# Kernel tuning notes

Hardware: AMD Instinct MI355X
Metric: run time of the kernel (lower is better)

Reference implementation:

```python
import jax, jax.numpy as jnp
import numpy as np

TAU = 2.0       # spikingjelly LIFNode default
V_TH = 1.0      # v_threshold default
ALPHA = 2.0     # surrogate.ATan default alpha

@jax.custom_vjp
def atan_spike(x):
    # Heaviside forward, ATan surrogate gradient backward
    return (x >= 0.0).astype(x.dtype)

def _atan_fwd(x):
    return atan_spike(x), x

def _atan_bwd(x, g):
    return (g * (ALPHA / 2.0) / (1.0 + (jnp.pi / 2.0 * ALPHA * x) ** 2),)

atan_spike.defvjp(_atan_fwd, _atan_bwd)

def lif_scan(cur):
    # cur: [T, ...]; LIF with decay_input=True, hard reset to v_reset=0
    def step(v, c):
        v = v + (c - v) / TAU          # charge with decayed input
        s = atan_spike(v - V_TH)       # fire
        v = (1.0 - s) * v              # hard reset (v_reset = 0)
        return v, s
    v0 = jnp.zeros(cur.shape[1:], cur.dtype)
    _, spikes = jax.lax.scan(step, v0, cur)
    return spikes

def setup_inputs() -> dict:
    key = jax.random.key(0)
    k1, k2 = jax.random.split(key, 2)
    T, B, D = 2048, 32, 512
    x = jax.random.normal(k1, (T, B, D), dtype=jnp.float32)
    W = jax.random.normal(k2, (D, D), dtype=jnp.float32) / np.sqrt(D).astype(np.float32)
    b = jnp.zeros((D,), dtype=jnp.float32)
    return {"x": x, "W": W, "b": b}

def reference(x, W, b):
    # x: [T, B, D]
    xs = jnp.stack([x, jnp.flip(x, axis=0)], axis=2)          # [T, B, 2, D]
    cur = jnp.einsum('tbkd,ed->tbke', xs, W) + b              # Linear (y = x W^T + b)
    s = lif_scan(cur)                                          # [T, B, 2, D] spikes
    return s[:, :, 0, :] + jnp.flip(s[:, :, 1, :], axis=0)    # [T, B, D]
```

## Files before the change

kernel.cpp:

```cpp
#include <hip/hip_runtime.h>
#include <cstddef>
#include <cstdint>

#define T_LEN 2048
#define B_SZ  32
#define D_SZ  512
#define BD    (B_SZ * D_SZ)

#define BM   128
#define BN   128

typedef const __attribute__((address_space(1))) uint32_t* gas1_t;
typedef __attribute__((address_space(3))) uint32_t* las3_t;

__global__ __launch_bounds__(256) void gemm8x8_kernel(
    const float* __restrict__ A,
    const float* __restrict__ W,
    const float* __restrict__ bias,
    float* __restrict__ Y)
{
#pragma clang fp contract(off)
  __shared__ float As[2][BM * 16];
  __shared__ float Bs[2][BN * 16];

  const int tid = threadIdx.x;
  const int tx  = tid & 15;
  const int ty  = tid >> 4;
  const int cA  = ty & 3;
  const int cB  = (tx >> 1) & 3;

  const int nwg  = (int)(gridDim.x * gridDim.y);
  const int orig = (int)(blockIdx.y * gridDim.x + blockIdx.x);
  const int q    = nwg >> 3, r = nwg & 7;
  const int xcd  = orig & 7, loc = orig >> 3;
  const int tix  = (xcd < r ? xcd * (q + 1) : r * (q + 1) + (xcd - r) * q) + loc;
  const int m0   = (tix >> 2) * BM;
  const int n0   = (tix & 3) * BN;

  const int lane  = tid & 63;
  const int wid   = tid >> 6;
  const int rloc  = lane >> 2;
  const int qA4   = (((lane & 3) ^ (rloc & 3)) << 2);
  const int qB4   = (((lane & 3) ^ ((rloc >> 1) & 3)) << 2);
  const int s0    = 2 * wid, s1 = 2 * wid + 1;
  const int oS0   = s0 * 256, oS1 = s1 * 256;
  const float* gA0 = A + (size_t)(m0 + s0 * 16 + rloc) * D_SZ + qA4;
  const float* gA1 = A + (size_t)(m0 + s1 * 16 + rloc) * D_SZ + qA4;
  const float* gB0 = W + (size_t)(n0 + s0 * 16 + rloc) * D_SZ + qB4;
  const float* gB1 = W + (size_t)(n0 + s1 * 16 + rloc) * D_SZ + qB4;

#define STAGE(BUF, KOFF)                                                      \
  do {                                                                        \
    __builtin_amdgcn_global_load_lds((gas1_t)(const void*)(gA0 + (KOFF)),     \
                                     (las3_t)(void*)(&As[BUF][oS0]), 16, 0, 0);\
    __builtin_amdgcn_global_load_lds((gas1_t)(const void*)(gA1 + (KOFF)),     \
                                     (las3_t)(void*)(&As[BUF][oS1]), 16, 0, 0);\
    __builtin_amdgcn_global_load_lds((gas1_t)(const void*)(gB0 + (KOFF)),     \
                                     (las3_t)(void*)(&Bs[BUF][oS0]), 16, 0, 0);\
    __builtin_amdgcn_global_load_lds((gas1_t)(const void*)(gB1 + (KOFF)),     \
                                     (las3_t)(void*)(&Bs[BUF][oS1]), 16, 0, 0);\
  } while (0)

  float acc[8][8];
#pragma unroll
  for (int i = 0; i < 8; ++i)
#pragma unroll
    for (int j = 0; j < 8; ++j) acc[i][j] = 0.0f;

  STAGE(0, 0);
  __syncthreads();

#pragma unroll 1
  for (int kc = 0; kc < 32; ++kc) {
    const int cur = kc & 1;
    if (kc + 1 < 32) STAGE(cur ^ 1, (kc + 1) * 16);

    const float* asb = &As[cur][0];
    const float* bsb = &Bs[cur][0];
#pragma unroll
    for (int kq = 0; kq < 4; ++kq) {
      const int bq = ((kq ^ cB) & 3) << 2;
      const int aq = ((kq ^ cA) & 3) << 2;
      float4 bfr[8];
#pragma unroll
      for (int j = 0; j < 8; ++j)
        bfr[j] = *(const float4*)&bsb[(tx + 16 * j) * 16 + bq];
#pragma unroll
      for (int i = 0; i < 8; ++i) {
        const float4 a = *(const float4*)&asb[(ty + 16 * i) * 16 + aq];
#pragma unroll
        for (int j = 0; j < 8; ++j) {
          acc[i][j] = fmaf(a.x, bfr[j].x, acc[i][j]);
          acc[i][j] = fmaf(a.y, bfr[j].y, acc[i][j]);
          acc[i][j] = fmaf(a.z, bfr[j].z, acc[i][j]);
          acc[i][j] = fmaf(a.w, bfr[j].w, acc[i][j]);
        }
      }
    }
    __syncthreads();
  }
#undef STAGE

#pragma unroll
  for (int i = 0; i < 8; ++i) {
    const int m = m0 + ty + 16 * i;
#pragma unroll
    for (int j = 0; j < 8; ++j) {
      const int n = n0 + tx + 16 * j;
      Y[(size_t)m * D_SZ + n] = acc[i][j] + bias[n];
    }
  }
}

#define CHK  16
#define CLEN 128

__global__ __launch_bounds__(64) void scan_chunk_kernel(
    const float* __restrict__ Y,
    float* __restrict__ out)
{
#pragma clang fp contract(off)
  const int idx = blockIdx.x * 64 + threadIdx.x;
  const int c   = blockIdx.y;
  const int t0  = c * CLEN;
  float ca[32], cb[32];
  uint32_t sf0, sf1, sf2, sf3, sb0, sb1, sb2, sb3;
  float v;

#define LD(R, TB)                                                             \
  _Pragma("unroll")                                                           \
  for (int j = 0; j < 32; ++j) R[j] = Y[(size_t)((TB) + j) * BD + idx];

#define FCH(R, W)                                                             \
  {                                                                           \
    uint32_t w_ = 0;                                                          \
    _Pragma("unroll")                                                         \
    for (int j = 0; j < 32; ++j) {                                            \
      v = v + (R[j] - v) * 0.5f;                                              \
      const bool s = (v - 1.0f) >= 0.0f;                                      \
      w_ |= (uint32_t)s << j;                                                 \
      v = s ? 0.0f : v;                                                       \
    }                                                                         \
    W = w_;                                                                   \
  }

#define BCH(R, W)                                                             \
  {                                                                           \
    uint32_t w_ = 0;                                                          \
    _Pragma("unroll")                                                         \
    for (int j = 31; j >= 0; --j) {                                           \
      v = v + (R[j] - v) * 0.5f;                                              \
      const bool s = (v - 1.0f) >= 0.0f;                                      \
      w_ |= (uint32_t)s << j;                                                 \
      v = s ? 0.0f : v;                                                       \
    }                                                                         \
    W = w_;                                                                   \
  }

  uint32_t wdump;

  v = 0.0f;
  if (c > 0) {
    LD(ca, t0 - 64)
    LD(cb, t0 - 32)
    FCH(ca, wdump)
    LD(ca, t0)
    FCH(cb, wdump)
  } else {
    LD(ca, t0)
  }
  LD(cb, t0 + 32)  FCH(ca, sf0)
  LD(ca, t0 + 64)  FCH(cb, sf1)
  LD(cb, t0 + 96)  FCH(ca, sf2)
                   FCH(cb, sf3)

  v = 0.0f;
  if (c < CHK - 1) {
    LD(ca, t0 + CLEN + 32)
    LD(cb, t0 + CLEN)
    BCH(ca, wdump)
    LD(ca, t0 + 96)
    BCH(cb, wdump)
  } else {
    LD(ca, t0 + 96)
  }
  LD(cb, t0 + 64)  BCH(ca, sb3)
  LD(ca, t0 + 32)  BCH(cb, sb2)
  LD(cb, t0)       BCH(ca, sb1)
                   BCH(cb, sb0)

#define WGRP(SF, SB, G)                                                       \
  _Pragma("unroll")                                                           \
  for (int j = 0; j < 32; ++j)                                                \
    out[(size_t)(t0 + (G) * 32 + j) * BD + idx] =                             \
        (float)(((SF >> j) & 1u) + ((SB >> j) & 1u));
  WGRP(sf0, sb0, 0) WGRP(sf1, sb1, 1) WGRP(sf2, sb2, 2) WGRP(sf3, sb3, 3)

#undef LD
#undef FCH
#undef BCH
#undef WGRP
}

__global__ __launch_bounds__(64) void lif_fwd_kernel(
    const float* __restrict__ Y, float* __restrict__ out,
    int tlen, float* __restrict__ vstate, int carry)
{
#pragma clang fp contract(off)
  const int idx = blockIdx.x * 64 + threadIdx.x;
  float v = carry ? vstate[idx] : 0.0f;
#pragma unroll 16
  for (int t = 0; t < tlen; ++t) {
    const float c = Y[(size_t)t * BD + idx];
    v = v + (c - v) * 0.5f;
    const bool s = (v - 1.0f) >= 0.0f;
    out[(size_t)t * BD + idx] = s ? 1.0f : 0.0f;
    v = s ? 0.0f : v;
  }
  vstate[idx] = v;
}

__global__ __launch_bounds__(64) void lif_bwd_kernel(
    const float* __restrict__ Y, float* __restrict__ out,
    int tlen, float* __restrict__ vstate, int carry)
{
#pragma clang fp contract(off)
  const int idx = blockIdx.x * 64 + threadIdx.x;
  float v = carry ? vstate[idx] : 0.0f;
#pragma unroll 16
  for (int tt = 0; tt < tlen; ++tt) {
    const size_t t = (size_t)(tlen - 1 - tt);
    const float c = Y[t * BD + idx];
    v = v + (c - v) * 0.5f;
    const bool s = (v - 1.0f) >= 0.0f;
    out[t * BD + idx] += s ? 1.0f : 0.0f;
    v = s ? 0.0f : v;
  }
  vstate[idx] = v;
}

extern "C" void kernel_launch(void* const* d_in, const int* in_sizes, int n_in,
                              void* d_out, int out_size, void* d_ws, size_t ws_size,
                              hipStream_t stream)
{
  const float* x = (const float*)d_in[0];
  const float* W = (const float*)d_in[1];
  const float* b = (const float*)d_in[2];
  float* out = (float*)d_out;

  const size_t full_bytes = (size_t)T_LEN * BD * sizeof(float);
  const size_t vbytes     = (size_t)BD * sizeof(float);

  if (ws_size >= full_bytes) {
    float* Y = (float*)d_ws;
    dim3 grid(T_LEN * B_SZ / BM, D_SZ / BN);
    gemm8x8_kernel<<<grid, 256, 0, stream>>>(x, W, b, Y);
    scan_chunk_kernel<<<dim3(BD / 64, CHK), 64, 0, stream>>>(Y, out);
  } else {
    const size_t avail = ws_size > vbytes ? ws_size - vbytes : 0;
    int Tc = T_LEN;
    while (Tc > 4 && (size_t)Tc * BD * sizeof(float) > avail) Tc >>= 1;
    float* Y      = (float*)d_ws;
    float* vstate = (float*)((char*)d_ws + (size_t)Tc * BD * sizeof(float));

    int first = 1;
    for (int t0 = 0; t0 < T_LEN; t0 += Tc) {
      dim3 grid(Tc * B_SZ / BM, D_SZ / BN);
      gemm8x8_kernel<<<grid, 256, 0, stream>>>(x + (size_t)t0 * BD, W, b, Y);
      lif_fwd_kernel<<<BD / 64, 64, 0, stream>>>(Y, out + (size_t)t0 * BD, Tc,
                                                 vstate, first ? 0 : 1);
      first = 0;
    }
    first = 1;
    for (int t0 = T_LEN - Tc; t0 >= 0; t0 -= Tc) {
      dim3 grid(Tc * B_SZ / BM, D_SZ / BN);
      gemm8x8_kernel<<<grid, 256, 0, stream>>>(x + (size_t)t0 * BD, W, b, Y);
      lif_bwd_kernel<<<BD / 64, 64, 0, stream>>>(Y, out + (size_t)t0 * BD, Tc,
                                                 vstate, first ? 0 : 1);
      first = 0;
    }
  }
}
```

Measured before the change: 650.2 us.

## Process two columns per thread with float2 loads and halve scan chunk length

The chunked LIF scan now has each thread handle two adjacent columns using float2 loads and stores, and the chunk length drops from 128 to 64 steps with twice as many chunks. The warm-up stays at 64 steps, so the redundant warm-up work grows relative to the useful work per chunk. The aim is wider memory transactions and two independent recurrences per thread for instruction-level parallelism. The cost is more redundant warm-up reads and higher register use.

```diff
diff --git a/kernel.cpp b/kernel.cpp
--- a/kernel.cpp
+++ b/kernel.cpp
@@ -112,94 +112,143 @@
   }
 }
 
-#define CHK  16
-#define CLEN 128
+#define CHK  32
+#define CLEN 64
 
 __global__ __launch_bounds__(64) void scan_chunk_kernel(
     const float* __restrict__ Y,
     float* __restrict__ out)
 {
 #pragma clang fp contract(off)
-  const int idx = blockIdx.x * 64 + threadIdx.x;
+  const int col = (blockIdx.x * 64 + threadIdx.x) * 2;
   const int c   = blockIdx.y;
   const int t0  = c * CLEN;
-  float ca[32], cb[32];
-  uint32_t sf0, sf1, sf2, sf3, sb0, sb1, sb2, sb3;
-  float v;
+  float2 ca[16], cb[16];
+  uint32_t sfx0, sfx1, sfy0, sfy1;
+  float vx, vy;
 
 #define LD(R, TB)                                                             \
   _Pragma("unroll")                                                           \
-  for (int j = 0; j < 32; ++j) R[j] = Y[(size_t)((TB) + j) * BD + idx];
-
-#define FCH(R, W)                                                             \
-  {                                                                           \
-    uint32_t w_ = 0;                                                          \
-    _Pragma("unroll")                                                         \
-    for (int j = 0; j < 32; ++j) {                                            \
-      v = v + (R[j] - v) * 0.5f;                                              \
-      const bool s = (v - 1.0f) >= 0.0f;                                      \
-      w_ |= (uint32_t)s << j;                                                 \
-      v = s ? 0.0f : v;                                                       \
-    }                                                                         \
-    W = w_;                                                                   \
-  }
-
-#define BCH(R, W)                                                             \
-  {                                                                           \
-    uint32_t w_ = 0;                                                          \
-    _Pragma("unroll")                                                         \
-    for (int j = 31; j >= 0; --j) {                                           \
-      v = v + (R[j] - v) * 0.5f;                                              \
-      const bool s = (v - 1.0f) >= 0.0f;                                      \
-      w_ |= (uint32_t)s << j;                                                 \
-      v = s ? 0.0f : v;                                                       \
-    }                                                                         \
-    W = w_;                                                                   \
-  }
-
-  uint32_t wdump;
-
-  v = 0.0f;
+  for (int j = 0; j < 16; ++j)                                                \
+    R[j] = *(const float2*)&Y[(size_t)((TB) + j) * BD + col];
+
+#define FW16(R)                                                               \
+  _Pragma("unroll")                                                           \
+  for (int j = 0; j < 16; ++j) {                                              \
+    vx = vx + (R[j].x - vx) * 0.5f;                                           \
+    const bool sx = (vx - 1.0f) >= 0.0f;                                      \
+    vx = sx ? 0.0f : vx;                                                      \
+    vy = vy + (R[j].y - vy) * 0.5f;                                           \
+    const bool sy = (vy - 1.0f) >= 0.0f;                                      \
+    vy = sy ? 0.0f : vy;                                                      \
+  }
+
+#define BW16(R)                                                               \
+  _Pragma("unroll")                                                           \
+  for (int j = 15; j >= 0; --j) {                                             \
+    vx = vx + (R[j].x - vx) * 0.5f;                                           \
+    const bool sx = (vx - 1.0f) >= 0.0f;                                      \
+    vx = sx ? 0.0f : vx;                                                      \
+    vy = vy + (R[j].y - vy) * 0.5f;                                           \
+    const bool sy = (vy - 1.0f) >= 0.0f;                                      \
+    vy = sy ? 0.0f : vy;                                                      \
+  }
+
+#define FCH16(R, BO)                                                          \
+  _Pragma("unroll")                                                           \
+  for (int j = 0; j < 16; ++j) {                                              \
+    vx = vx + (R[j].x - vx) * 0.5f;                                           \
+    const bool sx = (vx - 1.0f) >= 0.0f;                                      \
+    wx_ |= (uint32_t)sx << ((BO) + j);                                        \
+    vx = sx ? 0.0f : vx;                                                      \
+    vy = vy + (R[j].y - vy) * 0.5f;                                           \
+    const bool sy = (vy - 1.0f) >= 0.0f;                                      \
+    wy_ |= (uint32_t)sy << ((BO) + j);                                        \
+    vy = sy ? 0.0f : vy;                                                      \
+  }
+
+#define BCH16(R, BO)                                                          \
+  _Pragma("unroll")                                                           \
+  for (int j = 15; j >= 0; --j) {                                             \
+    vx = vx + (R[j].x - vx) * 0.5f;                                           \
+    const bool sx = (vx - 1.0f) >= 0.0f;                                      \
+    wx_ |= (uint32_t)sx << ((BO) + j);                                        \
+    vx = sx ? 0.0f : vx;                                                      \
+    vy = vy + (R[j].y - vy) * 0.5f;                                           \
+    const bool sy = (vy - 1.0f) >= 0.0f;                                      \
+    wy_ |= (uint32_t)sy << ((BO) + j);                                        \
+    vy = sy ? 0.0f : vy;                                                      \
+  }
+
+#define WR(SFX, SFY, G)                                                       \
+  _Pragma("unroll")                                                           \
+  for (int j = 0; j < 32; ++j) {                                              \
+    float2 rr;                                                                \
+    rr.x = (float)(((SFX >> j) & 1u) + ((wx_ >> j) & 1u));                    \
+    rr.y = (float)(((SFY >> j) & 1u) + ((wy_ >> j) & 1u));                    \
+    *(float2*)&out[(size_t)(t0 + (G) * 32 + j) * BD + col] = rr;              \
+  }
+
+  vx = 0.0f; vy = 0.0f;
   if (c > 0) {
     LD(ca, t0 - 64)
-    LD(cb, t0 - 32)
-    FCH(ca, wdump)
-    LD(ca, t0)
-    FCH(cb, wdump)
+    LD(cb, t0 - 48)
+    FW16(ca)  LD(ca, t0 - 32)
+    FW16(cb)  LD(cb, t0 - 16)
+    FW16(ca)  LD(ca, t0)
+    FW16(cb)
   } else {
     LD(ca, t0)
   }
-  LD(cb, t0 + 32)  FCH(ca, sf0)
-  LD(ca, t0 + 64)  FCH(cb, sf1)
-  LD(cb, t0 + 96)  FCH(ca, sf2)
-                   FCH(cb, sf3)
-
-  v = 0.0f;
+  {
+    uint32_t wx_ = 0, wy_ = 0;
+    LD(cb, t0 + 16)
+    FCH16(ca, 0)
+    LD(ca, t0 + 32)
+    FCH16(cb, 16)
+    sfx0 = wx_; sfy0 = wy_;
+  }
+  {
+    uint32_t wx_ = 0, wy_ = 0;
+    LD(cb, t0 + 48)
+    FCH16(ca, 0)
+    FCH16(cb, 16)
+    sfx1 = wx_; sfy1 = wy_;
+  }
+
+  vx = 0.0f; vy = 0.0f;
   if (c < CHK - 1) {
-    LD(ca, t0 + CLEN + 32)
-    LD(cb, t0 + CLEN)
-    BCH(ca, wdump)
-    LD(ca, t0 + 96)
-    BCH(cb, wdump)
+    LD(ca, t0 + CLEN + 48)
+    LD(cb, t0 + CLEN + 32)
+    BW16(ca)  LD(ca, t0 + CLEN + 16)
+    BW16(cb)  LD(cb, t0 + CLEN)
+    BW16(ca)  LD(ca, t0 + 48)
+    BW16(cb)
   } else {
-    LD(ca, t0 + 96)
-  }
-  LD(cb, t0 + 64)  BCH(ca, sb3)
-  LD(ca, t0 + 32)  BCH(cb, sb2)
-  LD(cb, t0)       BCH(ca, sb1)
-                   BCH(cb, sb0)
-
-#define WGRP(SF, SB, G)                                                       \
-  _Pragma("unroll")                                                           \
-  for (int j = 0; j < 32; ++j)                                                \
-    out[(size_t)(t0 + (G) * 32 + j) * BD + idx] =                             \
-        (float)(((SF >> j) & 1u) + ((SB >> j) & 1u));
-  WGRP(sf0, sb0, 0) WGRP(sf1, sb1, 1) WGRP(sf2, sb2, 2) WGRP(sf3, sb3, 3)
+    LD(ca, t0 + 48)
+  }
+  {
+    uint32_t wx_ = 0, wy_ = 0;
+    LD(cb, t0 + 32)
+    BCH16(ca, 16)
+    LD(ca, t0 + 16)
+    BCH16(cb, 0)
+    WR(sfx1, sfy1, 1)
+  }
+  {
+    uint32_t wx_ = 0, wy_ = 0;
+    LD(cb, t0)
+    BCH16(ca, 16)
+    BCH16(cb, 0)
+    WR(sfx0, sfy0, 0)
+  }
 
 #undef LD
-#undef FCH
-#undef BCH
-#undef WGRP
+#undef FW16
+#undef BW16
+#undef FCH16
+#undef BCH16
+#undef WR
 }
 
 __global__ __launch_bounds__(64) void lif_fwd_kernel(
@@ -255,7 +304,7 @@
     float* Y = (float*)d_ws;
     dim3 grid(T_LEN * B_SZ / BM, D_SZ / BN);
     gemm8x8_kernel<<<grid, 256, 0, stream>>>(x, W, b, Y);
-    scan_chunk_kernel<<<dim3(BD / 64, CHK), 64, 0, stream>>>(Y, out);
+    scan_chunk_kernel<<<dim3(BD / 128, CHK), 64, 0, stream>>>(Y, out);
   } else {
     const size_t avail = ws_size > vbytes ? ws_size - vbytes : 0;
     int Tc = T_LEN;
```

After: 701.4 us. 7.9% more time.
